# Performance work log

Measured on AMD Instinct MI355X. Metric: run time of the kernel, lower is better.

## Reference

```python
import jax, jax.numpy as jnp
import numpy as np

N_HEAD = 16
NEG_INF = -1e9


def setup_inputs() -> dict:
    key = jax.random.key(0)
    ks = jax.random.split(key, 5)
    B, T, C = 2, 2048, 1024
    scale = 1.0 / np.sqrt(C)
    return {
        "x": jax.random.normal(ks[0], (B, T, C), dtype=jnp.float32),
        "wq": jax.random.normal(ks[1], (C, C), dtype=jnp.float32) * scale,
        "bq": jnp.zeros((C,), dtype=jnp.float32),
        "wk": jax.random.normal(ks[2], (C, C), dtype=jnp.float32) * scale,
        "bk": jnp.zeros((C,), dtype=jnp.float32),
        "wv": jax.random.normal(ks[3], (C, C), dtype=jnp.float32) * scale,
        "bv": jnp.zeros((C,), dtype=jnp.float32),
        "wo": jax.random.normal(ks[4], (C, C), dtype=jnp.float32) * scale,
        "bo": jnp.zeros((C,), dtype=jnp.float32),
    }


def reference(x, wq, bq, wk, bk, wv, bv, wo, bo):
    B, T, C = x.shape
    H = N_HEAD
    d = C // H
    # linear projections, split into heads: [B, T, H, d]
    q = (x @ wq + bq).reshape(B, T, H, d)
    k = (x @ wk + bk).reshape(B, T, H, d)
    v = (x @ wv + bv).reshape(B, T, H, d)
    # scaled dot-product attention scores: [B, H, Tq, Tk]
    scores = jnp.einsum("bqhd,bkhd->bhqk", q, k) / jnp.sqrt(jnp.float32(d))
    # causal mask: triu(diagonal=1) positions are masked out
    causal = jnp.triu(jnp.ones((T, T), dtype=bool), k=1)
    scores = jnp.where(causal[None, None, :, :], NEG_INF, scores)
    attn = jax.nn.softmax(scores, axis=-1)
    # weighted values, merge heads: [B, T, C]
    out = jnp.einsum("bhqk,bkhd->bqhd", attn, v).reshape(B, T, C)
    # output projection (dropout is identity in eval / p=0)
    return out @ wo + bo
```

## Files before the change

kernel.cpp:

```cpp
#include <hip/hip_runtime.h>
#include <cstdint>
#include <type_traits>


#define TSEQ  2048
#define BATCH 2
#define CDIM  1024
#define NHEAD 16
#define DHEAD 64
#define NROWS (BATCH * TSEQ)

#define QSCALE 0.1803368801111244f

typedef unsigned short u16;
typedef u16   u16x8  __attribute__((ext_vector_type(8)));
typedef __bf16 bf16x8 __attribute__((ext_vector_type(8)));
typedef __bf16 bf16x2 __attribute__((ext_vector_type(2)));
typedef float f32x4  __attribute__((ext_vector_type(4)));

typedef const __attribute__((address_space(1))) void* gas_vp;
typedef __attribute__((address_space(3))) void* las_vp;

__device__ __forceinline__ u16 f2bf(float f) {
  return __builtin_bit_cast(u16, (__bf16)f);
}

__device__ __forceinline__ uint32_t pack2bf(float a, float b) {
  bf16x2 v;
  v[0] = (__bf16)a;
  v[1] = (__bf16)b;
  return __builtin_bit_cast(uint32_t, v);
}

__device__ __forceinline__ float max3f(float a, float b, float c) {
  return fmaxf(fmaxf(a, b), c);
}

__device__ __forceinline__ f32x4 mfma_bf16(u16x8 a, u16x8 b, f32x4 c) {
  return __builtin_amdgcn_mfma_f32_16x16x32_bf16(
      __builtin_bit_cast(bf16x8, a), __builtin_bit_cast(bf16x8, b), c, 0, 0, 0);
}

__device__ __forceinline__ void gload16(const u16* g, u16* l) {
  __builtin_amdgcn_global_load_lds((gas_vp)g, (las_vp)l, 16, 0, 0);
}


__global__ __launch_bounds__(256) void cast_x_kernel(const float* __restrict__ in,
                                                     u16* __restrict__ out, int n4) {
  int i = blockIdx.x * 256 + threadIdx.x;
  if (i < n4) {
    float4 v = ((const float4*)in)[i];
    ((uint2*)out)[i] = make_uint2(pack2bf(v.x, v.y), pack2bf(v.z, v.w));
  }
}

__global__ __launch_bounds__(256) void transpose_cast_kernel(
    const float* __restrict__ w0, const float* __restrict__ w1,
    const float* __restrict__ w2, const float* __restrict__ w3,
    u16* __restrict__ outQKV, u16* __restrict__ outO) {
  __shared__ float tile[32][33];
  const int m = blockIdx.z;
  const float* w = (m == 0) ? w0 : (m == 1) ? w1 : (m == 2) ? w2 : w3;
  const float scale = (m == 0) ? QSCALE : 1.0f;
  u16* out = (m < 3) ? (outQKV + (size_t)m * CDIM * CDIM) : outO;
  const int n0 = blockIdx.x * 32;
  const int k0 = blockIdx.y * 32;
  const int tx = threadIdx.x, ty = threadIdx.y;
#pragma unroll
  for (int i = 0; i < 4; ++i)
    tile[ty + i * 8][tx] = w[(size_t)(k0 + ty + i * 8) * CDIM + n0 + tx];
  __syncthreads();
#pragma unroll
  for (int i = 0; i < 4; ++i)
    out[(size_t)(n0 + ty + i * 8) * CDIM + k0 + tx] = f2bf(tile[tx][ty + i * 8] * scale);
}

__global__ __launch_bounds__(256) void bias_concat_kernel(const float* __restrict__ bq,
                                                          const float* __restrict__ bk,
                                                          const float* __restrict__ bv,
                                                          float* __restrict__ out) {
  int i = blockIdx.x * 256 + threadIdx.x;
  if (i < 3 * CDIM) {
    float v = (i < CDIM) ? bq[i] * QSCALE
            : (i < 2 * CDIM) ? bk[i - CDIM] : bv[i - 2 * CDIM];
    out[i] = v;
  }
}

__global__ __launch_bounds__(256) void vtrans_kernel(const u16* __restrict__ QKV,
                                                     u16* __restrict__ Vt) {
  __shared__ u16 tile[32][33];
  const int bh = blockIdx.z;
  const int b = bh >> 4, h = bh & 15;
  const int t0 = blockIdx.x * 32, d0 = blockIdx.y * 32;
  const int tx = threadIdx.x, ty = threadIdx.y;
#pragma unroll
  for (int i = 0; i < 4; ++i)
    tile[ty + i * 8][tx] =
        QKV[(size_t)(b * TSEQ + t0 + ty + i * 8) * (3 * CDIM) + 2 * CDIM + h * DHEAD + d0 + tx];
  __syncthreads();
#pragma unroll
  for (int i = 0; i < 4; ++i)
    Vt[(size_t)((b * NHEAD + h) * DHEAD + d0 + ty + i * 8) * TSEQ + t0 + tx] =
        tile[tx][ty + i * 8];
}


template <typename OutT>
__global__ __launch_bounds__(256) void gemm_bt_kernel(
    const u16* __restrict__ A, const u16* __restrict__ Bt,
    const float* __restrict__ bias, OutT* __restrict__ C,
    int M, int N, int K, int nb) {
  __shared__ u16 As[2][128 * 32];
  __shared__ u16 Bs[2][128 * 32];

  const int lid = blockIdx.x;
  const int x = lid & 7;
  const int xr = x & 3, xc = x >> 2;
  const int r = lid >> 3;
  const int nloc = r >> 3;
  const int mloc = r & 7;
  const int m0 = (xr * 8 + mloc) * 128;
  const int n0 = (xc * (nb >> 1) + nloc) * 128;

  const int t = threadIdx.x;
  const int lane = t & 63;
  const int w = t >> 6;
  const int wr = w >> 1, wc = w & 1;
  const int l15 = lane & 15;
  const int lg = lane >> 4;
  const int srow = lane >> 2;
  const int scol = (lane & 3) * 8;

  f32x4 acc[4][4];
#pragma unroll
  for (int i = 0; i < 4; ++i)
#pragma unroll
    for (int j = 0; j < 4; ++j) acc[i][j] = f32x4{0.f, 0.f, 0.f, 0.f};

  const int NK = K >> 5;

#pragma unroll
  for (int ci = 0; ci < 2; ++ci) {
    const int chunk = w * 2 + ci;
    const int grow = chunk * 16 + srow;
    gload16(&A[(size_t)(m0 + grow) * K + scol], &As[0][chunk * 512]);
    gload16(&Bt[(size_t)(n0 + grow) * K + scol], &Bs[0][chunk * 512]);
  }
  __syncthreads();

  for (int it = 0; it < NK; ++it) {
    const int cur = it & 1;
    if (it + 1 < NK) {
      const int k0 = (it + 1) * 32;
#pragma unroll
      for (int ci = 0; ci < 2; ++ci) {
        const int chunk = w * 2 + ci;
        const int grow = chunk * 16 + srow;
        gload16(&A[(size_t)(m0 + grow) * K + k0 + scol], &As[cur ^ 1][chunk * 512]);
        gload16(&Bt[(size_t)(n0 + grow) * K + k0 + scol], &Bs[cur ^ 1][chunk * 512]);
      }
    }
    u16x8 af[4], bf[4];
#pragma unroll
    for (int i = 0; i < 4; ++i)
      af[i] = *(const u16x8*)(&As[cur][(wr * 64 + i * 16 + l15) * 32 + lg * 8]);
#pragma unroll
    for (int j = 0; j < 4; ++j)
      bf[j] = *(const u16x8*)(&Bs[cur][(wc * 64 + j * 16 + l15) * 32 + lg * 8]);
    __builtin_amdgcn_s_setprio(1);
#pragma unroll
    for (int i = 0; i < 4; ++i)
#pragma unroll
      for (int j = 0; j < 4; ++j) acc[i][j] = mfma_bf16(af[i], bf[j], acc[i][j]);
    __builtin_amdgcn_s_setprio(0);
    __syncthreads();
  }

#pragma unroll
  for (int j = 0; j < 4; ++j) {
    int col = n0 + wc * 64 + j * 16 + l15;
    float bv = bias[col];
#pragma unroll
    for (int i = 0; i < 4; ++i) {
#pragma unroll
      for (int r2 = 0; r2 < 4; ++r2) {
        int row = m0 + wr * 64 + i * 16 + lg * 4 + r2;
        float val = acc[i][j][r2] + bv;
        if constexpr (std::is_same<OutT, float>::value)
          C[(size_t)row * N + col] = val;
        else
          C[(size_t)row * N + col] = f2bf(val);
      }
    }
  }
}


__global__ __launch_bounds__(256) void attn_kernel(const u16* __restrict__ QKV,
                                                   const u16* __restrict__ Vt,
                                                   u16* __restrict__ O) {
  __shared__ u16 Ks[2][64 * 64];
  __shared__ u16 Vs[2][64 * 64];
  __shared__ u16 Ps[4 * 16 * 64];

  const int t = threadIdx.x;
  const int lane = t & 63;
  const int w = t >> 6;
  const int l15 = lane & 15, lg = lane >> 4;
  const int xorv = (l15 & 7) << 4;

  const int lid = blockIdx.x;
  const int xcd = lid & 7;
  const int m = lid >> 3;
  const int bh = (m & 3) * 8 + xcd;
  const int qt = 31 - (m >> 2);
  const int b = bh >> 4, h = bh & 15;
  const int q0 = qt * 64;
  const int qrow = q0 + w * 16;
  const int nkt = qt + 1;

  const size_t RS = 3 * CDIM;
  const u16* Qp  = QKV + (size_t)(b * TSEQ) * RS + h * DHEAD;
  const u16* Kp  = Qp + CDIM;
  const u16* Vgp = Vt + (size_t)(b * NHEAD + h) * DHEAD * TSEQ;
  char* PwB = (char*)&Ps[w * 16 * 64];

  u16x8 qf[2];
#pragma unroll
  for (int c = 0; c < 2; ++c)
    qf[c] = *(const u16x8*)(&Qp[(size_t)(qrow + l15) * RS + c * 32 + lg * 8]);

  f32x4 acc[4];
#pragma unroll
  for (int g = 0; g < 4; ++g) acc[g] = f32x4{0.f, 0.f, 0.f, 0.f};
  float m_run = -3e38f, l_run = 0.f;

  const int sr = t >> 2;
  const int c2 = (t & 3) * 2;
  const int swA0 = sr * 128 + ((c2 * 16) ^ ((sr & 7) << 4));
  const int swA1 = sr * 128 + (((c2 + 1) * 16) ^ ((sr & 7) << 4));

  u16x8 kreg0 = *(const u16x8*)(&Kp[(size_t)sr * RS + c2 * 8]);
  u16x8 kreg1 = *(const u16x8*)(&Kp[(size_t)sr * RS + c2 * 8 + 8]);
  u16x8 vreg0 = *(const u16x8*)(&Vgp[(size_t)sr * TSEQ + c2 * 8]);
  u16x8 vreg1 = *(const u16x8*)(&Vgp[(size_t)sr * TSEQ + c2 * 8 + 8]);
  *(u16x8*)((char*)Ks[0] + swA0) = kreg0;
  *(u16x8*)((char*)Ks[0] + swA1) = kreg1;
  *(u16x8*)((char*)Vs[0] + swA0) = vreg0;
  *(u16x8*)((char*)Vs[0] + swA1) = vreg1;
  if (nkt > 1) {
    kreg0 = *(const u16x8*)(&Kp[(size_t)(64 + sr) * RS + c2 * 8]);
    kreg1 = *(const u16x8*)(&Kp[(size_t)(64 + sr) * RS + c2 * 8 + 8]);
    vreg0 = *(const u16x8*)(&Vgp[(size_t)sr * TSEQ + 64 + c2 * 8]);
    vreg1 = *(const u16x8*)(&Vgp[(size_t)sr * TSEQ + 64 + c2 * 8 + 8]);
  }
  __syncthreads();

  f32x4 sfr[4];
#pragma unroll
  for (int f = 0; f < 4; ++f) {
    const char* rowp = (char*)Ks[0] + (f * 16 + l15) * 128;
    u16x8 k0 = *(const u16x8*)(rowp + ((lg * 16) ^ xorv));
    u16x8 k1 = *(const u16x8*)(rowp + ((64 + lg * 16) ^ xorv));
    f32x4 s = mfma_bf16(k0, qf[0], f32x4{0.f, 0.f, 0.f, 0.f});
    sfr[f] = mfma_bf16(k1, qf[1], s);
  }

  for (int kb = 0; kb < nkt; ++kb) {
    const int p = kb & 1;
    char* VsB = (char*)Vs[p];

    if (kb + 1 < nkt) {
      *(u16x8*)((char*)Ks[p ^ 1] + swA0) = kreg0;
      *(u16x8*)((char*)Ks[p ^ 1] + swA1) = kreg1;
      *(u16x8*)((char*)Vs[p ^ 1] + swA0) = vreg0;
      *(u16x8*)((char*)Vs[p ^ 1] + swA1) = vreg1;
    }
    if (kb + 2 < nkt) {
      kreg0 = *(const u16x8*)(&Kp[(size_t)((kb + 2) * 64 + sr) * RS + c2 * 8]);
      kreg1 = *(const u16x8*)(&Kp[(size_t)((kb + 2) * 64 + sr) * RS + c2 * 8 + 8]);
      vreg0 = *(const u16x8*)(&Vgp[(size_t)sr * TSEQ + (kb + 2) * 64 + c2 * 8]);
      vreg1 = *(const u16x8*)(&Vgp[(size_t)sr * TSEQ + (kb + 2) * 64 + c2 * 8 + 8]);
    }
    __syncthreads();

    f32x4 snx[4];
    if (kb + 1 < nkt) {
      __builtin_amdgcn_s_setprio(1);
#pragma unroll
      for (int f = 0; f < 4; ++f) {
        const char* rowp = (char*)Ks[p ^ 1] + (f * 16 + l15) * 128;
        u16x8 k0 = *(const u16x8*)(rowp + ((lg * 16) ^ xorv));
        u16x8 k1 = *(const u16x8*)(rowp + ((64 + lg * 16) ^ xorv));
        f32x4 s = mfma_bf16(k0, qf[0], f32x4{0.f, 0.f, 0.f, 0.f});
        snx[f] = mfma_bf16(k1, qf[1], s);
      }
      __builtin_amdgcn_s_setprio(0);
    }

    if (kb * 64 + 63 > qrow) {
      const int q_abs = qrow + l15;
#pragma unroll
      for (int f = 0; f < 4; ++f) {
        const int kbase = kb * 64 + f * 16 + lg * 4;
#pragma unroll
        for (int r = 0; r < 4; ++r)
          if (kbase + r > q_abs) sfr[f][r] = -1e9f;
      }
    }

    float t0 = max3f(sfr[0][0], sfr[0][1], sfr[0][2]);
    float t1 = max3f(sfr[0][3], sfr[1][0], sfr[1][1]);
    float t2 = max3f(sfr[1][2], sfr[1][3], sfr[2][0]);
    float t3 = max3f(sfr[2][1], sfr[2][2], sfr[2][3]);
    float t4 = max3f(sfr[3][0], sfr[3][1], sfr[3][2]);
    float mx = fmaxf(max3f(t0, t1, t2), max3f(t3, t4, sfr[3][3]));

    if (__any(mx > m_run + 8.f)) {
      float gm = mx;
      gm = fmaxf(gm, __shfl_xor(gm, 16));
      gm = fmaxf(gm, __shfl_xor(gm, 32));
      float mnew = fmaxf(m_run, gm);
      float fac = exp2f(m_run - mnew);
      m_run = mnew;
      l_run *= fac;
#pragma unroll
      for (int g = 0; g < 4; ++g) acc[g] *= fac;
    }

    {
      char* pb = PwB + l15 * 128;
      float ls = 0.f;
#pragma unroll
      for (int f = 0; f < 4; ++f) {
        float p0 = exp2f(sfr[f][0] - m_run);
        float p1 = exp2f(sfr[f][1] - m_run);
        float p2 = exp2f(sfr[f][2] - m_run);
        float p3 = exp2f(sfr[f][3] - m_run);
        ls += (p0 + p1) + (p2 + p3);
        const int boff = (f * 32 + lg * 8) ^ xorv;
        *(uint2*)(pb + boff) = make_uint2(pack2bf(p0, p1), pack2bf(p2, p3));
      }
      l_run += ls;
    }

    __builtin_amdgcn_s_setprio(1);
#pragma unroll
    for (int c = 0; c < 2; ++c) {
      const int coff = (c * 64 + lg * 16) ^ xorv;
      u16x8 pf = *(const u16x8*)(PwB + l15 * 128 + coff);
#pragma unroll
      for (int g = 0; g < 4; ++g) {
        u16x8 vf = *(const u16x8*)(VsB + (g * 16 + l15) * 128 + coff);
        acc[g] = mfma_bf16(vf, pf, acc[g]);
      }
    }
    __builtin_amdgcn_s_setprio(0);

    __syncthreads();

#pragma unroll
    for (int f = 0; f < 4; ++f) sfr[f] = snx[f];
  }

  float lt = l_run;
  lt += __shfl_xor(lt, 16);
  lt += __shfl_xor(lt, 32);
  float inv = 1.f / lt;
  {
    char* pb = PwB + l15 * 128;
#pragma unroll
    for (int g = 0; g < 4; ++g) {
      const int boff = (g * 32 + lg * 8) ^ xorv;
      *(uint2*)(pb + boff) = make_uint2(pack2bf(acc[g][0] * inv, acc[g][1] * inv),
                                        pack2bf(acc[g][2] * inv, acc[g][3] * inv));
    }
  }
#pragma unroll
  for (int i = 0; i < 2; ++i) {
    const int rl = i * 8 + (lane >> 3);
    const int ch = lane & 7;
    u16x8 vv = *(const u16x8*)(PwB + rl * 128 + ((ch * 16) ^ ((rl & 7) << 4)));
    *(u16x8*)(&O[(size_t)(b * TSEQ + qrow + rl) * CDIM + h * DHEAD + ch * 8]) = vv;
  }
}


extern "C" void kernel_launch(void* const* d_in, const int* in_sizes, int n_in,
                              void* d_out, int out_size, void* d_ws, size_t ws_size,
                              hipStream_t stream) {
  const float* x  = (const float*)d_in[0];
  const float* wq = (const float*)d_in[1];
  const float* bq = (const float*)d_in[2];
  const float* wk = (const float*)d_in[3];
  const float* bk = (const float*)d_in[4];
  const float* wv = (const float*)d_in[5];
  const float* bv = (const float*)d_in[6];
  const float* wo = (const float*)d_in[7];
  const float* bo = (const float*)d_in[8];
  float* out = (float*)d_out;

  char* ws = (char*)d_ws;
  u16*  xb      = (u16*)(ws);
  u16*  Vtg     = (u16*)(ws);
  u16*  wqkvT   = (u16*)(ws + (8ll << 20));
  u16*  woT     = (u16*)(ws + (14ll << 20));
  u16*  QKV     = (u16*)(ws + (16ll << 20));
  u16*  Obuf    = (u16*)(ws + (40ll << 20));
  float* biasqkv = (float*)(ws + (48ll << 20));

  cast_x_kernel<<<(NROWS * CDIM / 4 + 255) / 256, 256, 0, stream>>>(x, xb, NROWS * CDIM / 4);
  {
    dim3 g(CDIM / 32, CDIM / 32, 4), blk(32, 8);
    transpose_cast_kernel<<<g, blk, 0, stream>>>(wq, wk, wv, wo, wqkvT, woT);
  }
  bias_concat_kernel<<<12, 256, 0, stream>>>(bq, bk, bv, biasqkv);
  gemm_bt_kernel<u16><<<(NROWS / 128) * ((3 * CDIM) / 128), 256, 0, stream>>>(
      xb, wqkvT, biasqkv, QKV, NROWS, 3 * CDIM, CDIM, (3 * CDIM) / 128);
  {
    dim3 g(TSEQ / 32, DHEAD / 32, BATCH * NHEAD), blk(32, 8);
    vtrans_kernel<<<g, blk, 0, stream>>>(QKV, Vtg);
  }
  attn_kernel<<<1024, 256, 0, stream>>>(QKV, Vtg, Obuf);
  gemm_bt_kernel<float><<<(NROWS / 128) * (CDIM / 128), 256, 0, stream>>>(
      Obuf, woT, bo, out, NROWS, CDIM, CDIM, CDIM / 128);
}
```

Baseline: 122.6 us.

## Use 256x256-tile, 512-thread GEMM kernel for fused QKV projection

Adds a new bf16 GEMM kernel with 256x256 output tiles, BK=64, 8 waves, XOR-swizzled LDS, and double-buffered global-to-LDS loads. These loads are interleaved with MFMA quadrants and use raised wave priority. It replaces the 128x128 GEMM for the QKV projection to raise arithmetic intensity and overlap loads with compute. The trade-offs are 128 KB of LDS per block and high register pressure. With only 192 workgroups on many CUs, occupancy and tail effects may suffer.

Measured after the change: 132.6 us. +8.2%, slower.

```diff
diff --git a/kernel.cpp b/kernel.cpp
--- a/kernel.cpp
+++ b/kernel.cpp
@@ -104,6 +104,127 @@
   for (int i = 0; i < 4; ++i)
     Vt[(size_t)((b * NHEAD + h) * DHEAD + d0 + ty + i * 8) * TSEQ + t0 + tx] =
         tile[tx][ty + i * 8];
+}
+
+
+__global__ __launch_bounds__(512) void gemm256_kernel(
+    const u16* __restrict__ A, const u16* __restrict__ Bt,
+    const float* __restrict__ bias, u16* __restrict__ C,
+    int M, int N, int K, int mb) {
+  __shared__ u16 As[2][256 * 64];
+  __shared__ u16 Bs[2][256 * 64];
+
+  const int lid = blockIdx.x;
+  const int nwg = gridDim.x;
+  const int swz = (lid & 7) * (nwg >> 3) + (lid >> 3);
+  const int m0 = (swz % mb) * 256;
+  const int n0 = (swz / mb) * 256;
+
+  const int t = threadIdx.x;
+  const int lane = t & 63;
+  const int w = t >> 6;
+  const int wr = w >> 2;
+  const int wc = w & 3;
+  const int l15 = lane & 15;
+  const int lg = lane >> 4;
+  const int xorv = (l15 & 7) << 4;
+
+  const int srow8 = lane >> 3;
+  const int scol_swz = ((((lane & 7) << 4) ^ (srow8 << 4)) >> 1);
+
+  f32x4 acc[8][4];
+#pragma unroll
+  for (int i = 0; i < 8; ++i)
+#pragma unroll
+    for (int j = 0; j < 4; ++j) acc[i][j] = f32x4{0.f, 0.f, 0.f, 0.f};
+
+  const int NK = K >> 6;
+
+#define STAGE256(buf, kt, rnd)                                                   \
+  {                                                                              \
+    const int c_ = (rnd) * 8 + w;                                                \
+    const int grow_ = c_ * 8 + srow8;                                            \
+    const int kk0_ = (kt) * 64;                                                  \
+    gload16(&A[(size_t)(m0 + grow_) * K + kk0_ + scol_swz], &As[buf][c_ * 512]); \
+    gload16(&Bt[(size_t)(n0 + grow_) * K + kk0_ + scol_swz], &Bs[buf][c_ * 512]);\
+  }
+
+#define LDA256(buf, mq, af)                                                      \
+  _Pragma("unroll") for (int mr_ = 0; mr_ < 4; ++mr_)                            \
+  _Pragma("unroll") for (int kk_ = 0; kk_ < 2; ++kk_)                            \
+    af[mr_ * 2 + kk_] = *(const u16x8*)((const char*)As[buf] +                   \
+        (wr * 128 + (mq) * 64 + mr_ * 16 + l15) * 128 +                          \
+        ((kk_ * 64 + lg * 16) ^ xorv));
+
+#define LDB256(buf, nh, bf)                                                      \
+  _Pragma("unroll") for (int j_ = 0; j_ < 2; ++j_)                               \
+  _Pragma("unroll") for (int kk_ = 0; kk_ < 2; ++kk_)                            \
+    bf[j_ * 2 + kk_] = *(const u16x8*)((const char*)Bs[buf] +                    \
+        (wc * 64 + (nh) * 32 + j_ * 16 + l15) * 128 +                            \
+        ((kk_ * 64 + lg * 16) ^ xorv));
+
+#define QUAD256(af, bf, mq, nh)                                                  \
+  __builtin_amdgcn_s_setprio(1);                                                 \
+  _Pragma("unroll") for (int mr_ = 0; mr_ < 4; ++mr_)                            \
+  _Pragma("unroll") for (int j_ = 0; j_ < 2; ++j_) {                             \
+    f32x4& a_ = acc[(mq) * 4 + mr_][(nh) * 2 + j_];                              \
+    a_ = mfma_bf16(af[mr_ * 2 + 0], bf[j_ * 2 + 0], a_);                         \
+    a_ = mfma_bf16(af[mr_ * 2 + 1], bf[j_ * 2 + 1], a_);                         \
+  }                                                                              \
+  __builtin_amdgcn_s_setprio(0);
+
+#pragma unroll
+  for (int r = 0; r < 4; ++r) STAGE256(0, 0, r);
+
+  for (int it = 0; it < NK; ++it) {
+    const int cur = it & 1;
+    const bool pf = (it + 1 < NK);
+    u16x8 af[8], bf[4];
+
+    if (pf) {
+      STAGE256(cur ^ 1, it + 1, 0);
+      asm volatile("s_waitcnt vmcnt(2)" ::: "memory");
+    } else {
+      asm volatile("s_waitcnt vmcnt(0)" ::: "memory");
+    }
+    __builtin_amdgcn_s_barrier();
+    __builtin_amdgcn_sched_barrier(0);
+    LDA256(cur, 0, af);
+    LDB256(cur, 0, bf);
+    QUAD256(af, bf, 0, 0);
+
+    if (pf) STAGE256(cur ^ 1, it + 1, 1);
+    LDA256(cur, 1, af);
+    QUAD256(af, bf, 1, 0);
+
+    if (pf) STAGE256(cur ^ 1, it + 1, 2);
+    LDB256(cur, 1, bf);
+    QUAD256(af, bf, 1, 1);
+
+    if (pf) STAGE256(cur ^ 1, it + 1, 3);
+    LDA256(cur, 0, af);
+    QUAD256(af, bf, 0, 1);
+
+    __builtin_amdgcn_s_barrier();
+    __builtin_amdgcn_sched_barrier(0);
+  }
+
+#pragma unroll
+  for (int jj = 0; jj < 4; ++jj) {
+    const int col = n0 + wc * 64 + (jj >> 1) * 32 + (jj & 1) * 16 + l15;
+    const float bv = bias[col];
+#pragma unroll
+    for (int i = 0; i < 8; ++i) {
+      const int rowb = m0 + wr * 128 + (i >> 2) * 64 + (i & 3) * 16 + lg * 4;
+#pragma unroll
+      for (int r = 0; r < 4; ++r)
+        C[(size_t)(rowb + r) * N + col] = f2bf(acc[i][jj][r] + bv);
+    }
+  }
+#undef STAGE256
+#undef LDA256
+#undef LDB256
+#undef QUAD256
 }
 
 
@@ -417,8 +538,8 @@
     transpose_cast_kernel<<<g, blk, 0, stream>>>(wq, wk, wv, wo, wqkvT, woT);
   }
   bias_concat_kernel<<<12, 256, 0, stream>>>(bq, bk, bv, biasqkv);
-  gemm_bt_kernel<u16><<<(NROWS / 128) * ((3 * CDIM) / 128), 256, 0, stream>>>(
-      xb, wqkvT, biasqkv, QKV, NROWS, 3 * CDIM, CDIM, (3 * CDIM) / 128);
+  gemm256_kernel<<<(NROWS / 256) * ((3 * CDIM) / 256), 512, 0, stream>>>(
+      xb, wqkvT, biasqkv, QKV, NROWS, 3 * CDIM, CDIM, NROWS / 256);
   {
     dim3 g(TSEQ / 32, DHEAD / 32, BATCH * NHEAD), blk(32, 8);
     vtrans_kernel<<<g, blk, 0, stream>>>(QKV, Vtg);
```
